# Kernel tuning notes

Measured on AMD Instinct MI355X. Metric: run time of the kernel, lower is better.

The kernel has to match this reference:

```python
import jax, jax.numpy as jnp
import numpy as np

HEADS = 4
DIM_HEAD = 32
EPS = 1e-5


def setup_inputs() -> dict:
    key = jax.random.key(0)
    ks = jax.random.split(key, 4)
    B, C, H, W = 4, 32, 32, 32
    hidden = C * HEADS * DIM_HEAD  # 4096
    image = jax.random.normal(ks[0], (B, C, H, W), dtype=jnp.float32)
    w_qkv = jax.random.normal(ks[1], (3 * hidden, C), dtype=jnp.float32) * (1.0 / np.sqrt(C))
    b_qkv = jnp.zeros((3 * hidden,), dtype=jnp.float32)
    w_out = jax.random.normal(ks[2], (C, hidden), dtype=jnp.float32) * (1.0 / np.sqrt(hidden))
    b_out = jnp.zeros((C,), dtype=jnp.float32)
    gn_gamma = jnp.ones((C,), dtype=jnp.float32)
    gn_beta = jnp.zeros((C,), dtype=jnp.float32)
    return {"image": image, "w_qkv": w_qkv, "b_qkv": b_qkv,
            "w_out": w_out, "b_out": b_out,
            "gn_gamma": gn_gamma, "gn_beta": gn_beta}


def reference(image, w_qkv, b_qkv, w_out, b_out, gn_gamma, gn_beta):
    B, C, H, W = image.shape
    hidden = C * HEADS * DIM_HEAD
    d = hidden // HEADS  # per-head channel dim = C * DIM_HEAD
    N = H * W
    scale = DIM_HEAD ** (-0.5)

    # 1x1 conv to qkv: [B, 3*hidden, H, W]
    qkv = jnp.einsum('bcxy,oc->boxy', image, w_qkv) + b_qkv[None, :, None, None]
    q, k, v = jnp.split(qkv, 3, axis=1)

    # einops 'b (c h) x y -> b h c (x y)': channel index = c*HEADS + h
    def rearr(t):
        return t.reshape(B, d, HEADS, N).transpose(0, 2, 1, 3)  # [B, h, d, N]

    q, k, v = rearr(q), rearr(k), rearr(v)

    q = jax.nn.softmax(q, axis=-2) * scale  # softmax over feature dim d
    k = jax.nn.softmax(k, axis=-1)          # softmax over spatial dim N

    context = jnp.einsum('bhdn,bhen->bhde', k, v)   # [B, h, d, d]
    out = jnp.einsum('bhde,bhdn->bhen', context, q)  # [B, h, d, N]

    # einops 'b h c (x y) -> b (h c) x y'
    out = out.reshape(B, hidden, H, W)

    # 1x1 conv back to channels, then GroupNorm(1, C)
    out = jnp.einsum('bcxy,oc->boxy', out, w_out) + b_out[None, :, None, None]
    mean = out.mean(axis=(1, 2, 3), keepdims=True)
    var = out.var(axis=(1, 2, 3), keepdims=True)
    out = (out - mean) * jax.lax.rsqrt(var + EPS)
    return out * gn_gamma[None, :, None, None] + gn_beta[None, :, None, None]
```

## Files before the change

### kernel.cpp

```cpp
#include <hip/hip_runtime.h>
#include <stdint.h>

#define HID 4096
#define NSP 1024
#define CIN 32

typedef unsigned short u16;
typedef float f32x4 __attribute__((ext_vector_type(4)));
typedef _Float16 f16;
typedef _Float16 f16x8 __attribute__((ext_vector_type(8)));
typedef unsigned short u16x4 __attribute__((ext_vector_type(4)));
typedef unsigned short u16x8 __attribute__((ext_vector_type(8)));

__device__ __forceinline__ u16 f2h(float f) {
  return __builtin_bit_cast(u16, (f16)f);
}
__device__ __forceinline__ float h2f(u16 u) {
  return (float)__builtin_bit_cast(f16, u);
}

__device__ __forceinline__ void gload16(const u16* g, u16* l) {
  __builtin_amdgcn_global_load_lds(
      (const __attribute__((address_space(1))) void*)g,
      (__attribute__((address_space(3))) void*)l, 16, 0, 0);
}

template <int SECBASE, bool DO_EXP>
__global__ __launch_bounds__(256) void conv_kv(const float* __restrict__ img,
    const float* __restrict__ wq, const float* __restrict__ bq,
    u16* __restrict__ out) {
  __shared__ __align__(16) float imgS[32 * 256];
  __shared__ __align__(16) float wS[32 * 64];
  __shared__ float bS[64];
  int t = threadIdx.x;
  int ch0 = blockIdx.x * 64, nt0 = blockIdx.y * 256, b = blockIdx.z;
  int nl = t & 63, cg = t >> 6;
#pragma unroll
  for (int i = 0; i < 8; i++) {
    int idx = t + i * 256;
    *(f32x4*)&imgS[idx * 4] =
        *(const f32x4*)&img[((size_t)b * CIN + (idx >> 6)) * NSP + nt0 + (idx & 63) * 4];
  }
#pragma unroll
  for (int i = 0; i < 8; i++) {
    int idx = t + i * 256;
    int chl = idx >> 5, c = idx & 31;
    wS[c * 64 + chl] = wq[(size_t)(SECBASE + ch0 + chl) * CIN + c];
  }
  if (t < 64) bS[t] = bq[SECBASE + ch0 + t];
  __syncthreads();
  f32x4 acc[16];
#pragma unroll
  for (int i = 0; i < 16; i++) {
    f32x4 zz = {0.f, 0.f, 0.f, 0.f};
    acc[i] = zz;
  }
#pragma unroll
  for (int c = 0; c < 32; c++) {
    f32x4 x = *(const f32x4*)&imgS[c * 256 + nl * 4];
    const f32x4* wv = (const f32x4*)&wS[c * 64 + cg * 16];
#pragma unroll
    for (int g = 0; g < 4; g++) {
      f32x4 w4 = wv[g];
      acc[g * 4 + 0] += w4[0] * x;
      acc[g * 4 + 1] += w4[1] * x;
      acc[g * 4 + 2] += w4[2] * x;
      acc[g * 4 + 3] += w4[3] * x;
    }
  }
#pragma unroll
  for (int i = 0; i < 16; i++) {
    int ch = ch0 + cg * 16 + i;
    float bias = bS[cg * 16 + i];
    u16x4 o;
#pragma unroll
    for (int j = 0; j < 4; j++) {
      float vv = acc[i][j] + bias;
      if constexpr (DO_EXP) vv = __expf(vv);
      o[j] = f2h(vv);
    }
    size_t row = (size_t)(b * 4 + (ch & 3)) * 1024 + (ch >> 2);
    *(u16x4*)&out[row * NSP + nt0 + nl * 4] = o;
  }
}

__global__ __launch_bounds__(256) void conv_q(const float* __restrict__ img,
    const float* __restrict__ wq, const float* __restrict__ bq,
    u16* __restrict__ qt) {
  __shared__ __align__(16) float imgS[32 * 256];
  __shared__ __align__(16) float wS[32 * 64];
  __shared__ float bS[64];
  int t = threadIdx.x;
  int d0 = blockIdx.x * 64, nt0 = blockIdx.y * 256, z = blockIdx.z;
  int b = z >> 2, hh = z & 3;
  int dl = t & 15, ng = t >> 4;
#pragma unroll
  for (int i = 0; i < 8; i++) {
    int idx = t + i * 256;
    *(f32x4*)&imgS[idx * 4] =
        *(const f32x4*)&img[((size_t)b * CIN + (idx >> 6)) * NSP + nt0 + (idx & 63) * 4];
  }
#pragma unroll
  for (int i = 0; i < 8; i++) {
    int idx = t + i * 256;
    int chl = idx >> 5, c = idx & 31;
    wS[c * 64 + chl] = wq[(size_t)((d0 + chl) * 4 + hh) * CIN + c];
  }
  if (t < 64) bS[t] = bq[(d0 + t) * 4 + hh];
  __syncthreads();
  f32x4 acc[16];
#pragma unroll
  for (int i = 0; i < 16; i++) {
    f32x4 zz = {0.f, 0.f, 0.f, 0.f};
    acc[i] = zz;
  }
#pragma unroll
  for (int c = 0; c < 32; c++) {
    f32x4 w4 = *(const f32x4*)&wS[c * 64 + dl * 4];
#pragma unroll
    for (int j = 0; j < 16; j++) {
      float x = imgS[c * 256 + ng + j * 16];
      acc[j] += x * w4;
    }
  }
  f32x4 bb = *(const f32x4*)&bS[dl * 4];
  size_t base = (size_t)z * 1024 * 1024;
#pragma unroll
  for (int j = 0; j < 16; j++) {
    int n = nt0 + ng + j * 16;
    u16x4 o;
#pragma unroll
    for (int q = 0; q < 4; q++) o[q] = f2h(__expf(acc[j][q] + bb[q]));
    *(u16x4*)&qt[base + (size_t)n * 1024 + d0 + dl * 4] = o;
  }
}

__global__ __launch_bounds__(256) void rowinv(const u16* __restrict__ kexp,
    const u16* __restrict__ qtexp, float* __restrict__ kinv,
    float* __restrict__ qinv) {
  int t = threadIdx.x;
  int wv = t >> 6, l = t & 63;
  int row = blockIdx.x * 4 + wv;
  const u16* src = (row < 16384) ? kexp + (size_t)row * 1024
                                 : qtexp + (size_t)(row - 16384) * 1024;
  const u16x8* p = (const u16x8*)(src + l * 16);
  u16x8 a = p[0], bvec = p[1];
  float s = 0.f;
#pragma unroll
  for (int j = 0; j < 8; j++) s += h2f(a[j]) + h2f(bvec[j]);
#pragma unroll
  for (int off = 32; off > 0; off >>= 1) s += __shfl_xor(s, off);
  if (l == 0) {
    s = fmaxf(s, 1e-20f);
    if (row < 16384) kinv[row] = 1.0f / s;
    else qinv[row - 16384] = 0.17677669529663687f / s;
  }
}

__global__ __launch_bounds__(256) void gemm_bt(const u16* __restrict__ A0,
    const u16* __restrict__ B0, u16* __restrict__ C0,
    const float* __restrict__ colscale) {
  __shared__ __align__(16) u16 As[2][128 * 64];
  __shared__ __align__(16) u16 Bs[2][128 * 64];
  int t = threadIdx.x;
  int w = t >> 6, l = t & 63;
  int bid = blockIdx.x;
  int xcd = bid & 7, rr = bid >> 3;
  int z = ((rr >> 6) << 3) | xcd;
  int by = (rr >> 3) & 7, bx = rr & 7;
  const u16* A = A0 + (size_t)z * (1024 * 1024) + (size_t)by * 128 * 1024;
  const u16* Bt = B0 + (size_t)z * (1024 * 1024) + (size_t)bx * 128 * 1024;
  int wr = w >> 1, wc = w & 1;
  f32x4 acc[4][4];
#pragma unroll
  for (int m = 0; m < 4; m++)
#pragma unroll
    for (int n = 0; n < 4; n++) {
      f32x4 zz = {0.f, 0.f, 0.f, 0.f};
      acc[m][n] = zz;
    }
  int srow = l >> 3;
  int scol = ((l & 7) ^ srow) * 8;
  auto STAGE = [&](int p, int k0) {
#pragma unroll
    for (int s = 0; s < 4; s++) {
      int strip = w * 4 + s;
      int r = strip * 8 + srow;
      gload16(A + (size_t)r * 1024 + k0 + scol, &As[p][strip * 512]);
      gload16(Bt + (size_t)r * 1024 + k0 + scol, &Bs[p][strip * 512]);
    }
  };
  auto COMPUTE = [&](int p) {
#pragma unroll
    for (int kk = 0; kk < 2; kk++) {
      f16x8 a[4], bb[4];
#pragma unroll
      for (int m = 0; m < 4; m++) {
        int row = wr * 64 + m * 16 + (l & 15);
        int idx = (kk * 32 + (l >> 4) * 8) ^ ((row & 7) * 8);
        a[m] = *(const f16x8*)&As[p][row * 64 + idx];
      }
#pragma unroll
      for (int n = 0; n < 4; n++) {
        int row = wc * 64 + n * 16 + (l & 15);
        int idx = (kk * 32 + (l >> 4) * 8) ^ ((row & 7) * 8);
        bb[n] = *(const f16x8*)&Bs[p][row * 64 + idx];
      }
#pragma unroll
      for (int m = 0; m < 4; m++)
#pragma unroll
        for (int n = 0; n < 4; n++)
          acc[m][n] = __builtin_amdgcn_mfma_f32_16x16x32_f16(a[m], bb[n], acc[m][n], 0, 0, 0);
    }
  };
  STAGE(0, 0);
  __syncthreads();
  for (int kt = 0; kt < 16; kt += 2) {
    STAGE(1, (kt + 1) * 64);
    COMPUTE(0);
    __syncthreads();
    if (kt + 2 < 16) STAGE(0, (kt + 2) * 64);
    COMPUTE(1);
    __syncthreads();
  }
  u16* Cp = C0 + (size_t)z * (1024 * 1024);
  const float* csz = colscale + (size_t)z * 1024;
  int rbase = by * 128 + wr * 64 + (l >> 4) * 4;
  int cbase = bx * 128 + wc * 64 + (l & 15);
  float sc[4];
#pragma unroll
  for (int n = 0; n < 4; n++) sc[n] = csz[cbase + n * 16];
#pragma unroll
  for (int m = 0; m < 4; m++)
#pragma unroll
    for (int n = 0; n < 4; n++)
#pragma unroll
      for (int j = 0; j < 4; j++) {
        int r = rbase + m * 16 + j;
        int cc = cbase + n * 16;
        Cp[(size_t)r * 1024 + cc] = f2h(acc[m][n][j] * sc[n]);
      }
}

__global__ __launch_bounds__(256) void oproj(const u16* __restrict__ att,
    const float* __restrict__ wout, float* __restrict__ partial) {
  __shared__ __align__(16) float wS[128 * 20];
  int t = threadIdx.x;
  int kc = blockIdx.x, og = blockIdx.y, b = blockIdx.z;
  for (int i = t; i < 128 * 16; i += 256) {
    int cc = i & 127, oo = i >> 7;
    wS[cc * 20 + oo] = wout[(size_t)(og * 16 + oo) * HID + kc * 128 + cc];
  }
  __syncthreads();
  f32x4 acc[16];
#pragma unroll
  for (int o = 0; o < 16; o++) {
    f32x4 zz = {0.f, 0.f, 0.f, 0.f};
    acc[o] = zz;
  }
  const u16* X = att + ((size_t)b * HID + kc * 128) * NSP + t * 4;
#pragma unroll 4
  for (int cc = 0; cc < 128; cc++) {
    u16x4 xr = *(const u16x4*)(X + (size_t)cc * NSP);
    f32x4 x = {h2f(xr[0]), h2f(xr[1]), h2f(xr[2]), h2f(xr[3])};
    const f32x4* wv = (const f32x4*)&wS[cc * 20];
#pragma unroll
    for (int g = 0; g < 4; g++) {
      f32x4 w4 = wv[g];
      acc[g * 4 + 0] += w4[0] * x;
      acc[g * 4 + 1] += w4[1] * x;
      acc[g * 4 + 2] += w4[2] * x;
      acc[g * 4 + 3] += w4[3] * x;
    }
  }
#pragma unroll
  for (int o = 0; o < 16; o++)
    *(f32x4*)&partial[(((size_t)b * 32 + kc) * 32 + og * 16 + o) * NSP + t * 4] = acc[o];
}

__global__ __launch_bounds__(256) void reduce_stats(const float* __restrict__ partial,
    const float* __restrict__ bout, float* __restrict__ fin,
    float* __restrict__ stats) {
  int t = threadIdx.x;
  int gid = blockIdx.x * 256 + t;
  int n = gid & 1023;
  int o = (gid >> 10) & 31;
  int b = gid >> 15;
  const float* p = partial + ((size_t)b * 32 * 32 + o) * NSP + n;
  float v[32];
#pragma unroll
  for (int kc = 0; kc < 32; kc++) v[kc] = p[(size_t)kc * 32 * NSP];
  float s = bout[o];
#pragma unroll
  for (int kc = 0; kc < 32; kc++) s += v[kc];
  fin[((size_t)b * 32 + o) * NSP + n] = s;
  float s1 = s, s2 = s * s;
#pragma unroll
  for (int off = 32; off > 0; off >>= 1) {
    s1 += __shfl_xor(s1, off);
    s2 += __shfl_xor(s2, off);
  }
  __shared__ float r1[4], r2[4];
  int wid = t >> 6;
  if ((t & 63) == 0) { r1[wid] = s1; r2[wid] = s2; }
  __syncthreads();
  if (t == 0) {
    stats[blockIdx.x * 2 + 0] = r1[0] + r1[1] + r1[2] + r1[3];
    stats[blockIdx.x * 2 + 1] = r2[0] + r2[1] + r2[2] + r2[3];
  }
}

__global__ __launch_bounds__(256) void gn_norm(const float* __restrict__ fin,
    const float* __restrict__ stats, const float* __restrict__ gamma,
    const float* __restrict__ beta, float* __restrict__ out) {
  int t = threadIdx.x;
  int nc = blockIdx.x, b = blockIdx.y;
  float s1 = 0.f, s2 = 0.f;
  for (int i = 0; i < 128; i++) {
    s1 += stats[(b * 128 + i) * 2 + 0];
    s2 += stats[(b * 128 + i) * 2 + 1];
  }
  const float inv_n = 1.0f / 32768.0f;
  float mean = s1 * inv_n;
  float var = s2 * inv_n - mean * mean;
  float rstd = rsqrtf(var + 1e-5f);
  int nl = t & 63, oq = t >> 6;
  int n = nc * 64 + nl;
#pragma unroll
  for (int oo = 0; oo < 8; oo++) {
    int o = oq * 8 + oo;
    float v = fin[((size_t)b * 32 + o) * NSP + n];
    out[((size_t)b * 32 + o) * NSP + n] = (v - mean) * rstd * gamma[o] + beta[o];
  }
}

extern "C" void kernel_launch(void* const* d_in, const int* in_sizes, int n_in,
                              void* d_out, int out_size, void* d_ws, size_t ws_size,
                              hipStream_t stream) {
  (void)in_sizes; (void)n_in; (void)out_size; (void)ws_size;
  const float* img   = (const float*)d_in[0];
  const float* wqkv  = (const float*)d_in[1];
  const float* bqkv  = (const float*)d_in[2];
  const float* wout  = (const float*)d_in[3];
  const float* bout  = (const float*)d_in[4];
  const float* gamma = (const float*)d_in[5];
  const float* beta  = (const float*)d_in[6];
  char* ws = (char*)d_ws;
  u16*   v       = (u16*)(ws + 0);
  u16*   att     = (u16*)(ws + 0);
  u16*   kexp    = (u16*)(ws + 33554432);
  u16*   qtexp   = (u16*)(ws + 67108864);
  u16*   ctx     = (u16*)(ws + 100663296);
  float* stats   = (float*)(ws + 100663296);
  float* partial = (float*)(ws + 134217728);
  float* kinv    = (float*)(ws + 134217728);
  float* qinv    = (float*)(ws + 134283264);
  float* fin     = (float*)(ws + 150994944);
  float* out = (float*)d_out;

  conv_kv<2 * HID, false><<<dim3(64, 4, 4), 256, 0, stream>>>(img, wqkv, bqkv, v);
  conv_kv<1 * HID, true ><<<dim3(64, 4, 4), 256, 0, stream>>>(img, wqkv, bqkv, kexp);
  conv_q<<<dim3(16, 4, 16), 256, 0, stream>>>(img, wqkv, bqkv, qtexp);
  rowinv<<<dim3(8192), 256, 0, stream>>>(kexp, qtexp, kinv, qinv);
  gemm_bt<<<dim3(1024), 256, 0, stream>>>(v, kexp, ctx, kinv);
  gemm_bt<<<dim3(1024), 256, 0, stream>>>(ctx, qtexp, att, qinv);
  oproj<<<dim3(32, 2, 4), 256, 0, stream>>>(att, wout, partial);
  reduce_stats<<<dim3(512), 256, 0, stream>>>(partial, bout, fin, stats);
  gn_norm<<<dim3(16, 4), 256, 0, stream>>>(fin, stats, gamma, beta, out);
}
```

Measured before the change: 214.3 us.

## Replace 128x128 batched GEMM with 256x256 8-wave pipelined tile kernel

The batched fp16 MFMA GEMM used for the context and attention products moves from 128x128 tiles with 4 waves to 256x256 tiles with 8 waves. Global-to-LDS loads are split into half-tile stages interleaved between four MFMA phases, with explicit vmcnt waits, sched barriers and s_setprio around the MFMA bursts. The larger tile halves global and LDS traffic per FLOP, and the finer staging is meant to overlap loads with compute. In exchange it uses more LDS (128KB per block), more accumulator registers, and only 256 blocks, which may hurt occupancy and load balance across CUs.

After: 206.0 us (median of 2 runs). 3.9% less time.

```diff
diff --git a/kernel.cpp b/kernel.cpp
--- a/kernel.cpp
+++ b/kernel.cpp
@@ -157,89 +157,144 @@
   }
 }
 
-__global__ __launch_bounds__(256) void gemm_bt(const u16* __restrict__ A0,
+template <int MB, bool FIRST>
+__device__ __forceinline__ void phase_load(int wm, int wn, int l,
+    const u16* ASp, const u16* BSp, f16x8 (&bfr)[4][2], f16x8 (&afr)[2][2]) {
+  if constexpr (FIRST) {
+#pragma unroll
+    for (int n = 0; n < 4; n++) {
+      int row = wn * 64 + n * 16 + (l & 15);
+#pragma unroll
+      for (int ks = 0; ks < 2; ks++) {
+        int cjs = (ks * 4 + (l >> 4)) ^ (row & 7);
+        bfr[n][ks] = *(const f16x8*)&BSp[row * 64 + cjs * 8];
+      }
+    }
+  }
+#pragma unroll
+  for (int mm = 0; mm < 2; mm++) {
+    int row = wm * 128 + (MB + mm) * 16 + (l & 15);
+#pragma unroll
+    for (int ks = 0; ks < 2; ks++) {
+      int cjs = (ks * 4 + (l >> 4)) ^ (row & 7);
+      afr[mm][ks] = *(const f16x8*)&ASp[row * 64 + cjs * 8];
+    }
+  }
+}
+
+template <int MB>
+__device__ __forceinline__ void phase_fma(f16x8 (&bfr)[4][2], f16x8 (&afr)[2][2],
+                                          f32x4 (&acc)[8][4]) {
+  __builtin_amdgcn_s_setprio(1);
+#pragma unroll
+  for (int n = 0; n < 4; n++) {
+#pragma unroll
+    for (int mm = 0; mm < 2; mm++) {
+      acc[MB + mm][n] = __builtin_amdgcn_mfma_f32_16x16x32_f16(
+          afr[mm][0], bfr[n][0], acc[MB + mm][n], 0, 0, 0);
+      acc[MB + mm][n] = __builtin_amdgcn_mfma_f32_16x16x32_f16(
+          afr[mm][1], bfr[n][1], acc[MB + mm][n], 0, 0, 0);
+    }
+  }
+  __builtin_amdgcn_s_setprio(0);
+}
+
+#define SCHED0 __builtin_amdgcn_sched_barrier(0)
+#define BARRIER() do { SCHED0; __builtin_amdgcn_s_barrier(); SCHED0; } while (0)
+
+__global__ __launch_bounds__(512, 2) void gemm8(const u16* __restrict__ A0,
     const u16* __restrict__ B0, u16* __restrict__ C0,
     const float* __restrict__ colscale) {
-  __shared__ __align__(16) u16 As[2][128 * 64];
-  __shared__ __align__(16) u16 Bs[2][128 * 64];
+  __shared__ __align__(16) u16 AS[2][256 * 64];
+  __shared__ __align__(16) u16 BS[2][256 * 64];
   int t = threadIdx.x;
   int w = t >> 6, l = t & 63;
+  int wm = w >> 2, wn = w & 3;
   int bid = blockIdx.x;
   int xcd = bid & 7, rr = bid >> 3;
-  int z = ((rr >> 6) << 3) | xcd;
-  int by = (rr >> 3) & 7, bx = rr & 7;
-  const u16* A = A0 + (size_t)z * (1024 * 1024) + (size_t)by * 128 * 1024;
-  const u16* Bt = B0 + (size_t)z * (1024 * 1024) + (size_t)bx * 128 * 1024;
-  int wr = w >> 1, wc = w & 1;
-  f32x4 acc[4][4];
-#pragma unroll
-  for (int m = 0; m < 4; m++)
+  int z = ((rr >> 4) << 3) | xcd;
+  int ti = rr & 15, by = ti >> 2, bx = ti & 3;
+  const u16* Ag = A0 + (size_t)z * (1024 * 1024) + (size_t)by * 256 * 1024;
+  const u16* Bg = B0 + (size_t)z * (1024 * 1024) + (size_t)bx * 256 * 1024;
+
+  f32x4 acc[8][4];
+#pragma unroll
+  for (int m = 0; m < 8; m++)
 #pragma unroll
     for (int n = 0; n < 4; n++) {
       f32x4 zz = {0.f, 0.f, 0.f, 0.f};
       acc[m][n] = zz;
     }
-  int srow = l >> 3;
-  int scol = ((l & 7) ^ srow) * 8;
-  auto STAGE = [&](int p, int k0) {
-#pragma unroll
-    for (int s = 0; s < 4; s++) {
-      int strip = w * 4 + s;
-      int r = strip * 8 + srow;
-      gload16(A + (size_t)r * 1024 + k0 + scol, &As[p][strip * 512]);
-      gload16(Bt + (size_t)r * 1024 + k0 + scol, &Bs[p][strip * 512]);
+  f16x8 bfr[4][2];
+
+  auto stageH = [&](u16* lds, const u16* g, int half, int k0) {
+#pragma unroll
+    for (int i = 0; i < 2; i++) {
+      int cid = i * 512 + t;
+      int r = cid >> 3, cj = cid & 7;
+      gload16(g + (size_t)(half * 128 + r) * 1024 + k0 + ((cj ^ (r & 7)) * 8),
+              lds + (half * 128 + r) * 64 + cj * 8);
     }
   };
-  auto COMPUTE = [&](int p) {
-#pragma unroll
-    for (int kk = 0; kk < 2; kk++) {
-      f16x8 a[4], bb[4];
-#pragma unroll
-      for (int m = 0; m < 4; m++) {
-        int row = wr * 64 + m * 16 + (l & 15);
-        int idx = (kk * 32 + (l >> 4) * 8) ^ ((row & 7) * 8);
-        a[m] = *(const f16x8*)&As[p][row * 64 + idx];
-      }
-#pragma unroll
-      for (int n = 0; n < 4; n++) {
-        int row = wc * 64 + n * 16 + (l & 15);
-        int idx = (kk * 32 + (l >> 4) * 8) ^ ((row & 7) * 8);
-        bb[n] = *(const f16x8*)&Bs[p][row * 64 + idx];
-      }
-#pragma unroll
-      for (int m = 0; m < 4; m++)
-#pragma unroll
-        for (int n = 0; n < 4; n++)
-          acc[m][n] = __builtin_amdgcn_mfma_f32_16x16x32_f16(a[m], bb[n], acc[m][n], 0, 0, 0);
-    }
-  };
-  STAGE(0, 0);
-  __syncthreads();
-  for (int kt = 0; kt < 16; kt += 2) {
-    STAGE(1, (kt + 1) * 64);
-    COMPUTE(0);
-    __syncthreads();
-    if (kt + 2 < 16) STAGE(0, (kt + 2) * 64);
-    COMPUTE(1);
-    __syncthreads();
-  }
+
+  stageH(BS[0], Bg, 0, 0);
+  stageH(BS[0], Bg, 1, 0);
+  stageH(AS[0], Ag, 0, 0);
+  stageH(AS[0], Ag, 1, 0);
+  stageH(BS[1], Bg, 0, 64);
+  stageH(BS[1], Bg, 1, 64);
+  stageH(AS[1], Ag, 0, 64);
+  asm volatile("s_waitcnt vmcnt(6)" ::: "memory");
+  BARRIER();
+
+  for (int kt = 0; kt < 16; kt++) {
+    int pb = kt & 1;
+    const u16* ASp = AS[pb];
+    const u16* BSp = BS[pb];
+    int kN1 = (kt + 1) * 64, kN2 = (kt + 2) * 64;
+    f16x8 afr[2][2];
+    phase_load<0, true>(wm, wn, l, ASp, BSp, bfr, afr);
+    if (kt < 15) stageH(AS[1 - pb], Ag, 1, kN1);
+    BARRIER();
+    phase_fma<0>(bfr, afr, acc);
+    BARRIER();
+    phase_load<2, false>(wm, wn, l, ASp, BSp, bfr, afr);
+    if (kt < 14) stageH(BS[pb], Bg, 0, kN2);
+    BARRIER();
+    phase_fma<2>(bfr, afr, acc);
+    BARRIER();
+    phase_load<4, false>(wm, wn, l, ASp, BSp, bfr, afr);
+    if (kt < 14) stageH(BS[pb], Bg, 1, kN2);
+    BARRIER();
+    phase_fma<4>(bfr, afr, acc);
+    BARRIER();
+    phase_load<6, false>(wm, wn, l, ASp, BSp, bfr, afr);
+    BARRIER();
+    phase_fma<6>(bfr, afr, acc);
+    BARRIER();
+    if (kt < 14) stageH(AS[pb], Ag, 0, kN2);
+    if (kt < 15) {
+      if (kt == 14) asm volatile("s_waitcnt vmcnt(0)" ::: "memory");
+      else          asm volatile("s_waitcnt vmcnt(6)" ::: "memory");
+      BARRIER();
+    }
+  }
+
   u16* Cp = C0 + (size_t)z * (1024 * 1024);
   const float* csz = colscale + (size_t)z * 1024;
-  int rbase = by * 128 + wr * 64 + (l >> 4) * 4;
-  int cbase = bx * 128 + wc * 64 + (l & 15);
+  int rbase = by * 256 + wm * 128 + (l >> 4) * 4;
+  int cbase = bx * 256 + wn * 64 + (l & 15);
   float sc[4];
 #pragma unroll
   for (int n = 0; n < 4; n++) sc[n] = csz[cbase + n * 16];
 #pragma unroll
-  for (int m = 0; m < 4; m++)
+  for (int m = 0; m < 8; m++)
 #pragma unroll
     for (int n = 0; n < 4; n++)
 #pragma unroll
-      for (int j = 0; j < 4; j++) {
-        int r = rbase + m * 16 + j;
-        int cc = cbase + n * 16;
-        Cp[(size_t)r * 1024 + cc] = f2h(acc[m][n][j] * sc[n]);
-      }
+      for (int j = 0; j < 4; j++)
+        Cp[(size_t)(rbase + m * 16 + j) * 1024 + cbase + n * 16] =
+            f2h(acc[m][n][j] * sc[n]);
 }
 
 __global__ __launch_bounds__(256) void oproj(const u16* __restrict__ att,
@@ -362,8 +417,8 @@
   conv_kv<1 * HID, true ><<<dim3(64, 4, 4), 256, 0, stream>>>(img, wqkv, bqkv, kexp);
   conv_q<<<dim3(16, 4, 16), 256, 0, stream>>>(img, wqkv, bqkv, qtexp);
   rowinv<<<dim3(8192), 256, 0, stream>>>(kexp, qtexp, kinv, qinv);
-  gemm_bt<<<dim3(1024), 256, 0, stream>>>(v, kexp, ctx, kinv);
-  gemm_bt<<<dim3(1024), 256, 0, stream>>>(ctx, qtexp, att, qinv);
+  gemm8<<<dim3(256), 512, 0, stream>>>(v, kexp, ctx, kinv);
+  gemm8<<<dim3(256), 512, 0, stream>>>(ctx, qtexp, att, qinv);
   oproj<<<dim3(32, 2, 4), 256, 0, stream>>>(att, wout, partial);
   reduce_stats<<<dim3(512), 256, 0, stream>>>(partial, bout, fin, stats);
   gn_norm<<<dim3(16, 4), 256, 0, stream>>>(fin, stats, gamma, beta, out);
```
